# Optimization experiments

Hardware: AMD Instinct MI355X
Metric: run time of the kernel (lower is better)

The kernel has to match this reference:

```python
import jax, jax.numpy as jnp
from jax import lax
import numpy as np

IN_F, CELL, OUT_F = 1024, 1024, 1024
B, T = 128, 256


def setup_inputs() -> dict:
    key = jax.random.key(0)
    ks = jax.random.split(key, 12)
    s_gate = 1.0 / np.sqrt(IN_F + CELL)
    s_cls = 1.0 / np.sqrt(CELL)
    d = {
        "x": jax.random.normal(ks[0], (B, T, IN_F), jnp.float32),
        "Wf": jax.random.normal(ks[1], (CELL + IN_F, CELL), jnp.float32) * s_gate,
        "bf": jax.random.normal(ks[2], (CELL,), jnp.float32) * s_gate,
        "Wi1": jax.random.normal(ks[3], (CELL + IN_F, CELL), jnp.float32) * s_gate,
        "bi1": jax.random.normal(ks[4], (CELL,), jnp.float32) * s_gate,
        "Wi2": jax.random.normal(ks[5], (CELL + IN_F, CELL), jnp.float32) * s_gate,
        "bi2": jax.random.normal(ks[6], (CELL,), jnp.float32) * s_gate,
        "Wo": jax.random.normal(ks[7], (CELL + IN_F, CELL), jnp.float32) * s_gate,
        "bo": jax.random.normal(ks[8], (CELL,), jnp.float32) * s_gate,
        "Wc": jax.random.normal(ks[9], (CELL, OUT_F), jnp.float32) * s_cls,
        "bc": jax.random.normal(ks[10], (OUT_F,), jnp.float32) * s_cls,
    }
    return d


def reference(x, Wf, bf, Wi1, bi1, Wi2, bi2, Wo, bo, Wc, bc):
    # x: [B, T, IN_F]
    Bsz, Tlen, _ = x.shape
    H = Wf.shape[1]
    xt = jnp.transpose(x, (1, 0, 2))  # [T, B, IN_F], matches x.permute(1,0,2)

    def step(cell, x_i):
        # concat order matches torch.cat((cell_state, x[i]), dim=2)
        inp = jnp.concatenate([cell, x_i], axis=-1)  # [B, H + IN_F]
        f = jax.nn.sigmoid(inp @ Wf + bf)
        cell1 = cell * f
        i1 = jax.nn.sigmoid(inp @ Wi1 + bi1)
        i2 = jnp.tanh(inp @ Wi2 + bi2)
        cell2 = cell1 + i1 * i2
        o1 = jax.nn.sigmoid(inp @ Wo + bo)
        h = o1 * jnp.tanh(cell2)
        out = h @ Wc + bc  # [B, OUT_F]
        return cell2, out

    c0 = jnp.zeros((Bsz, H), x.dtype)
    c_final, outs = lax.scan(step, c0, xt)  # outs: [T, B, OUT_F]
    output_sequence = jnp.transpose(outs, (1, 0, 2))  # [B, T, OUT_F]
    return output_sequence, c_final[None, :, :]  # cell_state kept as [1, B, H]
```

## Files before the change

### kernel.cpp

```cpp
#include <hip/hip_runtime.h>
#include <cstdint>
#include <cstddef>

#define DEVINL __device__ __forceinline__

typedef __attribute__((ext_vector_type(8))) short bf16x8;
typedef __attribute__((ext_vector_type(4))) float f32x4;
typedef __attribute__((ext_vector_type(4))) unsigned short u16x4;
typedef __attribute__((ext_vector_type(4))) unsigned int u32x4;

static constexpr size_t OFF_XB   = 0;
static constexpr size_t OFF_WHT  = OFF_XB  + (size_t)32768*1024*2;
static constexpr size_t OFF_WXT  = OFF_WHT + (size_t)4096*1024*2;
static constexpr size_t OFF_WCT  = OFF_WXT + (size_t)4096*1024*2;
static constexpr size_t OFF_BIAS = OFF_WCT + (size_t)1024*1024*2;
static constexpr size_t OFF_XW   = OFF_BIAS + 4096*4;
static constexpr size_t OFF_H    = OFF_XW  + (size_t)32768*4096*2;
static constexpr size_t OFF_CB   = OFF_H   + (size_t)32768*1024*2;
static constexpr size_t OFF_BAR  = OFF_CB  + (size_t)2*128*1024*2;
static constexpr size_t WS_NEEDED = OFF_BAR + 32768;

DEVINL unsigned short f2b(float f) {
  union { float f; unsigned u; } v; v.f = f;
  unsigned r = (v.u + 0x7FFFu + ((v.u >> 16) & 1u)) >> 16;
  return (unsigned short)r;
}
DEVINL float b2f(unsigned short h) {
  union { unsigned u; float f; } v; v.u = ((unsigned)h) << 16;
  return v.f;
}
DEVINL float sigmoidf_(float x) { return 1.0f / (1.0f + __expf(-x)); }
DEVINL float tanhf_(float x) { float e = __expf(2.0f * x); return 1.0f - 2.0f / (e + 1.0f); }
DEVINL f32x4 MFMA(bf16x8 a, bf16x8 b, f32x4 c) {
  return __builtin_amdgcn_mfma_f32_16x16x32_bf16(a, b, c, 0, 0, 0);
}
DEVINL void gload16(const void* g, void* l) {
  __builtin_amdgcn_global_load_lds(
      (const __attribute__((address_space(1))) void*)g,
      (__attribute__((address_space(3))) void*)l, 16, 0, 0);
}

__global__ void cvt_x_kernel(const float* __restrict__ x, unsigned short* __restrict__ xb) {
  size_t i = ((size_t)blockIdx.x * 256 + threadIdx.x) * 4;
  float4 v = *(const float4*)(x + i);
  u16x4 o; o.x = f2b(v.x); o.y = f2b(v.y); o.z = f2b(v.z); o.w = f2b(v.w);
  *(u16x4*)(xb + i) = o;
}

__global__ __launch_bounds__(256)
void cvt_w_kernel(const float* __restrict__ Wf, const float* __restrict__ Wi1,
                  const float* __restrict__ Wi2, const float* __restrict__ Wo,
                  unsigned short* __restrict__ WhT, unsigned short* __restrict__ WxT) {
  __shared__ float tile[64][65];
  const int bid = blockIdx.x;
  const int g  = bid & 3;
  const int kt = (bid >> 2) & 15;
  const int jt = bid >> 6;
  const float* W = (g == 0) ? Wf : (g == 1) ? Wi1 : (g == 2) ? Wi2 : Wo;
  const int tid = threadIdx.x;
  const int jj  = tid & 63;
  const int kr  = tid >> 6;

  for (int h = 0; h < 2; ++h) {
    const float* Wb = W + (size_t)(h ? 1024 : 0) * 1024;
#pragma unroll
    for (int i = 0; i < 16; ++i) {
      int kl = i * 4 + kr;
      tile[kl][jj] = Wb[(size_t)(kt * 64 + kl) * 1024 + jt * 64 + jj];
    }
    __syncthreads();
    unsigned short* Out = h ? WxT : WhT;
    unsigned short* op  = Out + (size_t)(4 * (jt * 64 + jj) + g) * 1024 + kt * 64 + kr * 16;
#pragma unroll
    for (int q = 0; q < 4; ++q) {
      u16x4 v;
#pragma unroll
      for (int e = 0; e < 4; ++e)
        ((unsigned short*)&v)[e] = f2b(tile[kr * 16 + q * 4 + e][jj]);
      *(u16x4*)(op + q * 4) = v;
    }
    __syncthreads();
  }
}

__global__ void bias_kernel(const float* __restrict__ bf_, const float* __restrict__ bi1,
                            const float* __restrict__ bi2, const float* __restrict__ bo,
                            float* __restrict__ biasAll) {
  int gc = blockIdx.x * 256 + threadIdx.x;
  int j = gc >> 2, g = gc & 3;
  const float* bb = (g == 0) ? bf_ : (g == 1) ? bi1 : (g == 2) ? bi2 : bo;
  biasAll[gc] = bb[j];
}

__global__ void cvt_wc_kernel(const float* __restrict__ Wc, unsigned short* __restrict__ WcT) {
  int idx = blockIdx.x * 256 + threadIdx.x;
  int k = idx & 1023, n = idx >> 10;
  WcT[idx] = f2b(Wc[(size_t)k * 1024 + n]);
}

template<bool OUT_F32>
__global__ __launch_bounds__(512, 2)
void gemm_bt(const unsigned short* __restrict__ A,
             const unsigned short* __restrict__ Bt,
             const float* __restrict__ bias,
             void* __restrict__ C,
             int M, int N, int K) {
  __shared__ char sT[4][32768];
  const int tid  = threadIdx.x;
  const int lane = tid & 63;
  const int wid  = tid >> 6;
  const int wm   = (wid >> 2) * 128;
  const int wn   = (wid & 3) * 64;

  const int nwg = gridDim.x * gridDim.y;
  const int lin = blockIdx.y * gridDim.x + blockIdx.x;
  const int cpx = nwg >> 3;
  const int swz = (lin & 7) * cpx + (lin >> 3);
  const int m0  = (swz / gridDim.x) * 256;
  const int n0  = (swz % gridDim.x) * 256;

  const int nt = K >> 5;

  f32x4 acc[8][4];
#pragma unroll
  for (int i = 0; i < 8; ++i)
#pragma unroll
    for (int j = 0; j < 4; ++j) acc[i][j] = (f32x4){0.f, 0.f, 0.f, 0.f};

  auto stageA = [&](int kt, int buf) {
#pragma unroll
    for (int l = 0; l < 2; ++l) {
      int s = l * 512 + tid;
      int r = s >> 2, c = s & 3;
      int cg = c ^ ((r >> 1) & 3);
      gload16(A + (size_t)(m0 + r) * K + kt * 32 + cg * 8, sT[buf] + s * 16);
    }
  };
  auto stageB = [&](int kt, int buf) {
#pragma unroll
    for (int l = 0; l < 2; ++l) {
      int s = l * 512 + tid;
      int r = s >> 2, c = s & 3;
      int cg = c ^ ((r >> 1) & 3);
      gload16(Bt + (size_t)(n0 + r) * K + kt * 32 + cg * 8, sT[buf] + 16384 + s * 16);
    }
  };

  stageA(0, 0); stageB(0, 0);
  stageA(1, 1); stageB(1, 1);
  stageA(2, 2); stageB(2, 2);
  asm volatile("s_waitcnt vmcnt(8)" ::: "memory");
  __builtin_amdgcn_s_barrier();

  const int ch = lane >> 4;

#pragma unroll 1
  for (int g = 0; g < nt; ++g) {
    const int rb = g & 3;
    const char* ab = sT[rb];
    const char* bb = sT[rb] + 16384;

    bf16x8 bv[4], av[4];
#pragma unroll
    for (int ni = 0; ni < 4; ++ni) {
      int col = wn + ni * 16 + (lane & 15);
      bv[ni] = *(const bf16x8*)(bb + col * 64 + ((ch ^ ((col >> 1) & 3)) << 4));
    }
#pragma unroll
    for (int mi = 0; mi < 4; ++mi) {
      int row = wm + mi * 16 + (lane & 15);
      av[mi] = *(const bf16x8*)(ab + row * 64 + ((ch ^ ((row >> 1) & 3)) << 4));
    }
    if (g + 3 < nt) stageA(g + 3, (g + 3) & 3);
    __builtin_amdgcn_s_barrier();
    __builtin_amdgcn_s_setprio(1);
#pragma unroll
    for (int mi = 0; mi < 4; ++mi)
#pragma unroll
      for (int ni = 0; ni < 4; ++ni)
        acc[mi][ni] = MFMA(av[mi], bv[ni], acc[mi][ni]);
    __builtin_amdgcn_s_setprio(0);
    __builtin_amdgcn_s_barrier();

#pragma unroll
    for (int mi = 0; mi < 4; ++mi) {
      int row = wm + 64 + mi * 16 + (lane & 15);
      av[mi] = *(const bf16x8*)(ab + row * 64 + ((ch ^ ((row >> 1) & 3)) << 4));
    }
    if (g + 3 < nt) stageB(g + 3, (g + 3) & 3);
    __builtin_amdgcn_s_barrier();
    __builtin_amdgcn_s_setprio(1);
#pragma unroll
    for (int mi = 0; mi < 4; ++mi)
#pragma unroll
      for (int ni = 0; ni < 4; ++ni)
        acc[mi + 4][ni] = MFMA(av[mi], bv[ni], acc[mi + 4][ni]);
    __builtin_amdgcn_s_setprio(0);

    if (g <= nt - 4)      asm volatile("s_waitcnt vmcnt(8)" ::: "memory");
    else if (g == nt - 3) asm volatile("s_waitcnt vmcnt(4)" ::: "memory");
    else if (g == nt - 2) asm volatile("s_waitcnt vmcnt(0)" ::: "memory");
    __builtin_amdgcn_s_barrier();
  }

#pragma unroll
  for (int mi = 0; mi < 8; ++mi)
#pragma unroll
    for (int ni = 0; ni < 4; ++ni)
#pragma unroll
      for (int r = 0; r < 4; ++r) {
        int row = m0 + wm + mi * 16 + (lane >> 4) * 4 + r;
        int col = n0 + wn + ni * 16 + (lane & 15);
        float v = acc[mi][ni][r] + bias[col];
        if (OUT_F32) ((float*)C)[(size_t)row * N + col] = v;
        else ((unsigned short*)C)[(size_t)row * N + col] = f2b(v);
      }
}

__global__ __launch_bounds__(512, 2)
void lstm_persist(const unsigned short* __restrict__ WhT,
                  const unsigned short* __restrict__ XW,
                  unsigned short* __restrict__ H,
                  unsigned short* __restrict__ cB0,
                  unsigned short* __restrict__ cB1,
                  float* __restrict__ cellOut,
                  unsigned* __restrict__ bar) {
  __shared__ __align__(16) char  sA[16 * 2064];
  __shared__ __align__(16) float sP[16 * 132];

  const int tid  = threadIdx.x;
  const int lane = tid & 63;
  const int nh   = tid >> 6;
  const int wgid = blockIdx.x;
  const int mq   = wgid & 7;
  const int cs   = wgid >> 3;
  const int sg   = cs >> 2;

  unsigned* qc   = bar + mq * 64;
  unsigned* qf   = bar + 512 + mq * 64;
  unsigned* gcnt = bar + 1024 + (mq * 8 + sg) * 64;

  const int r0 = lane & 15;
  const int ch = lane >> 4;

  bf16x8 bfr[32];
  {
    const unsigned short* bp = WhT + (size_t)(cs * 128 + nh * 16 + r0) * 1024 + ch * 8;
#pragma unroll
    for (int ks = 0; ks < 32; ++ks)
      bfr[ks] = *(const volatile bf16x8*)(bp + ks * 32);
  }

  const int b_local = (tid & 255) >> 4;
  const int jp      = (tid & 15) * 2;
  const int browg   = mq * 16 + b_local;
  float cf0 = 0.f, cf1 = 0.f;

  const unsigned short* xwp = XW + (size_t)browg * 256 * 4096 + cs * 128 + jp * 4;
  unsigned* c0p = (unsigned*)(cB0 + (size_t)browg * 1024 + cs * 32 + jp);
  unsigned* c1p = (unsigned*)(cB1 + (size_t)browg * 1024 + cs * 32 + jp);
  unsigned short* hp = H + (size_t)browg * 256 * 1024 + cs * 32 + jp;

  const int strow = tid >> 7;
  const int stcc  = tid & 127;

  for (int t = 0; t < 256; ++t) {
    const unsigned short* cinq = ((t & 1) ? cB1 : cB0) + (size_t)mq * 16 * 1024;

    bf16x8 xw;
    if (tid < 256) xw = *(const bf16x8*)(xwp + (size_t)t * 4096);

    u32x4 st[4];
#pragma unroll
    for (int it = 0; it < 4; ++it) {
      const void* p = cinq + (size_t)(it * 4 + strow) * 1024 + stcc * 8;
      asm volatile("global_load_dwordx4 %0, %1, off sc0 sc1"
                   : "=&v"(st[it]) : "v"(p) : "memory");
    }
    asm volatile("s_waitcnt vmcnt(0)" ::: "memory");
    __builtin_amdgcn_sched_barrier(0);
#pragma unroll
    for (int it = 0; it < 4; ++it) {
      int r = it * 4 + strow;
      *(u32x4*)&sA[r * 2064 + stcc * 16] = st[it];
    }
    __syncthreads();

    f32x4 acc = (f32x4){0.f, 0.f, 0.f, 0.f};
#pragma unroll
    for (int ks = 0; ks < 32; ++ks) {
      bf16x8 a0 = *(const bf16x8*)&sA[r0 * 2064 + (ch + ks * 4) * 16];
      acc = MFMA(a0, bfr[ks], acc);
    }

#pragma unroll
    for (int rr = 0; rr < 4; ++rr)
      sP[(ch * 4 + rr) * 132 + nh * 16 + r0] = acc[rr];
    __syncthreads();

    if (tid < 256) {
      float4 g0 = *(const float4*)&sP[b_local * 132 + jp * 4];
      float4 g1 = *(const float4*)&sP[b_local * 132 + jp * 4 + 4];

      float c2a, c2b, ha, hb;
      {
        float pf = g0.x + b2f((unsigned short)xw[0]);
        float pi = g0.y + b2f((unsigned short)xw[1]);
        float pg = g0.z + b2f((unsigned short)xw[2]);
        float po = g0.w + b2f((unsigned short)xw[3]);
        float f = sigmoidf_(pf), i1 = sigmoidf_(pi), gg = tanhf_(pg), o = sigmoidf_(po);
        c2a = cf0 * f + i1 * gg; cf0 = c2a; ha = o * tanhf_(c2a);
      }
      {
        float pf = g1.x + b2f((unsigned short)xw[4]);
        float pi = g1.y + b2f((unsigned short)xw[5]);
        float pg = g1.z + b2f((unsigned short)xw[6]);
        float po = g1.w + b2f((unsigned short)xw[7]);
        float f = sigmoidf_(pf), i1 = sigmoidf_(pi), gg = tanhf_(pg), o = sigmoidf_(po);
        c2b = cf1 * f + i1 * gg; cf1 = c2b; hb = o * tanhf_(c2b);
      }

      unsigned cw = (unsigned)f2b(c2a) | ((unsigned)f2b(c2b) << 16);
      __hip_atomic_store((t & 1) ? c0p : c1p, cw,
                         __ATOMIC_RELAXED, __HIP_MEMORY_SCOPE_AGENT);
      unsigned hw = (unsigned)f2b(ha) | ((unsigned)f2b(hb) << 16);
      *(unsigned*)(hp + (size_t)t * 1024) = hw;
    }

    __syncthreads();
    if (tid == 0) {
      unsigned tgt1 = 4u * (unsigned)(t + 1);
      unsigned tgt2 = 8u * (unsigned)(t + 1);
      unsigned n = __hip_atomic_fetch_add(gcnt, 1u, __ATOMIC_RELAXED,
                                          __HIP_MEMORY_SCOPE_AGENT);
      if (n == tgt1 - 1u) {
        unsigned m = __hip_atomic_fetch_add(qc, 1u, __ATOMIC_RELAXED,
                                            __HIP_MEMORY_SCOPE_AGENT);
        if (m == tgt2 - 1u)
          __hip_atomic_store(qf, (unsigned)(t + 1),
                             __ATOMIC_RELAXED, __HIP_MEMORY_SCOPE_AGENT);
      }
      while (__hip_atomic_load(qf, __ATOMIC_RELAXED, __HIP_MEMORY_SCOPE_AGENT)
             < (unsigned)(t + 1))
        __builtin_amdgcn_s_sleep(1);
    }
    __syncthreads();
  }

  if (tid < 256)
    *(float2*)(cellOut + (size_t)browg * 1024 + cs * 32 + jp) = make_float2(cf0, cf1);
}

extern "C" void kernel_launch(void* const* d_in, const int* in_sizes, int n_in,
                              void* d_out, int out_size, void* d_ws, size_t ws_size,
                              hipStream_t stream) {
  const float* x   = (const float*)d_in[0];
  const float* Wf  = (const float*)d_in[1];
  const float* bfv = (const float*)d_in[2];
  const float* Wi1 = (const float*)d_in[3];
  const float* bi1 = (const float*)d_in[4];
  const float* Wi2 = (const float*)d_in[5];
  const float* bi2 = (const float*)d_in[6];
  const float* Wo  = (const float*)d_in[7];
  const float* bo  = (const float*)d_in[8];
  const float* Wc  = (const float*)d_in[9];
  const float* bc  = (const float*)d_in[10];
  float* out = (float*)d_out;

  if (ws_size < WS_NEEDED) return;

  char* ws = (char*)d_ws;
  unsigned short* xb      = (unsigned short*)(ws + OFF_XB);
  unsigned short* WhT     = (unsigned short*)(ws + OFF_WHT);
  unsigned short* WxT     = (unsigned short*)(ws + OFF_WXT);
  unsigned short* WcT     = (unsigned short*)(ws + OFF_WCT);
  float*          biasAll = (float*)(ws + OFF_BIAS);
  unsigned short* XW      = (unsigned short*)(ws + OFF_XW);
  unsigned short* H       = (unsigned short*)(ws + OFF_H);
  unsigned short* cB0     = (unsigned short*)(ws + OFF_CB);
  unsigned short* cB1     = (unsigned short*)(ws + OFF_CB + (size_t)128 * 1024 * 2);
  unsigned*       barLn   = (unsigned*)(ws + OFF_BAR);
  float*          cellOut = out + (size_t)32768 * 1024;

  hipMemsetAsync(cB0, 0, (size_t)128 * 1024 * 2, stream);
  hipMemsetAsync(barLn, 0, 32768, stream);

  cvt_x_kernel <<<32768, 256, 0, stream>>>(x, xb);
  cvt_w_kernel <<< 1024, 256, 0, stream>>>(Wf, Wi1, Wi2, Wo, WhT, WxT);
  bias_kernel  <<<   16, 256, 0, stream>>>(bfv, bi1, bi2, bo, biasAll);
  cvt_wc_kernel<<< 4096, 256, 0, stream>>>(Wc, WcT);

  gemm_bt<false><<<dim3(16, 128), 512, 0, stream>>>(xb, WxT, biasAll, XW, 32768, 4096, 1024);

  {
    void* args[] = { (void*)&WhT, (void*)&XW, (void*)&H,
                     (void*)&cB0, (void*)&cB1, (void*)&cellOut, (void*)&barLn };
    hipLaunchCooperativeKernel(lstm_persist, dim3(256), dim3(512), args, 0u, stream);
  }

  gemm_bt<true><<<dim3(4, 128), 512, 0, stream>>>(H, WcT, bc, out, 32768, 1024, 1024);
}
```

Baseline: 1.415 ms.

## Spread gate epilogue over all threads and overlap output-gate work with barrier

The elementwise gate epilogue now uses all 512 threads, one cell column each, instead of 256 threads handling two columns. Packed bf16 cell and h stores are rebuilt with lane shuffles. The output-gate and h computation and the next step's XW prefetch are moved between the barrier arrive and the spin-wait, so they run off the recurrence's critical path. This shortens the serial per-step epilogue before the cross-workgroup barrier, at the cost of extra shuffles and some register pressure.

```diff
diff --git a/kernel.cpp b/kernel.cpp
--- a/kernel.cpp
+++ b/kernel.cpp
@@ -251,24 +251,23 @@
       bfr[ks] = *(const volatile bf16x8*)(bp + ks * 32);
   }
 
-  const int b_local = (tid & 255) >> 4;
-  const int jp      = (tid & 15) * 2;
-  const int browg   = mq * 16 + b_local;
-  float cf0 = 0.f, cf1 = 0.f;
-
-  const unsigned short* xwp = XW + (size_t)browg * 256 * 4096 + cs * 128 + jp * 4;
-  unsigned* c0p = (unsigned*)(cB0 + (size_t)browg * 1024 + cs * 32 + jp);
-  unsigned* c1p = (unsigned*)(cB1 + (size_t)browg * 1024 + cs * 32 + jp);
-  unsigned short* hp = H + (size_t)browg * 256 * 1024 + cs * 32 + jp;
+  const int erow  = tid >> 5;
+  const int ecol  = tid & 31;
+  const int browg = mq * 16 + erow;
+  float cf = 0.f;
+
+  const unsigned short* xwp = XW + (size_t)browg * 256 * 4096 + cs * 128 + ecol * 4;
+  unsigned* c0p = (unsigned*)(cB0 + (size_t)browg * 1024 + cs * 32 + ecol);
+  unsigned* c1p = (unsigned*)(cB1 + (size_t)browg * 1024 + cs * 32 + ecol);
+  unsigned* hp  = (unsigned*)(H + (size_t)browg * 256 * 1024 + cs * 32 + ecol);
 
   const int strow = tid >> 7;
   const int stcc  = tid & 127;
 
+  u16x4 xw = *(const u16x4*)(xwp);
+
   for (int t = 0; t < 256; ++t) {
     const unsigned short* cinq = ((t & 1) ? cB1 : cB0) + (size_t)mq * 16 * 1024;
-
-    bf16x8 xw;
-    if (tid < 256) xw = *(const bf16x8*)(xwp + (size_t)t * 4096);
 
     u32x4 st[4];
 #pragma unroll
@@ -298,34 +297,18 @@
       sP[(ch * 4 + rr) * 132 + nh * 16 + r0] = acc[rr];
     __syncthreads();
 
-    if (tid < 256) {
-      float4 g0 = *(const float4*)&sP[b_local * 132 + jp * 4];
-      float4 g1 = *(const float4*)&sP[b_local * 132 + jp * 4 + 4];
-
-      float c2a, c2b, ha, hb;
-      {
-        float pf = g0.x + b2f((unsigned short)xw[0]);
-        float pi = g0.y + b2f((unsigned short)xw[1]);
-        float pg = g0.z + b2f((unsigned short)xw[2]);
-        float po = g0.w + b2f((unsigned short)xw[3]);
-        float f = sigmoidf_(pf), i1 = sigmoidf_(pi), gg = tanhf_(pg), o = sigmoidf_(po);
-        c2a = cf0 * f + i1 * gg; cf0 = c2a; ha = o * tanhf_(c2a);
-      }
-      {
-        float pf = g1.x + b2f((unsigned short)xw[4]);
-        float pi = g1.y + b2f((unsigned short)xw[5]);
-        float pg = g1.z + b2f((unsigned short)xw[6]);
-        float po = g1.w + b2f((unsigned short)xw[7]);
-        float f = sigmoidf_(pf), i1 = sigmoidf_(pi), gg = tanhf_(pg), o = sigmoidf_(po);
-        c2b = cf1 * f + i1 * gg; cf1 = c2b; hb = o * tanhf_(c2b);
-      }
-
-      unsigned cw = (unsigned)f2b(c2a) | ((unsigned)f2b(c2b) << 16);
-      __hip_atomic_store((t & 1) ? c0p : c1p, cw,
+    float4 g = *(const float4*)&sP[erow * 132 + ecol * 4];
+    float pf = g.x + b2f((unsigned short)xw[0]);
+    float pi = g.y + b2f((unsigned short)xw[1]);
+    float pg = g.z + b2f((unsigned short)xw[2]);
+    float f  = sigmoidf_(pf), i1 = sigmoidf_(pi), gg = tanhf_(pg);
+    float c2 = cf * f + i1 * gg; cf = c2;
+
+    unsigned cl = f2b(c2);
+    unsigned chi = __shfl_down(cl, 1);
+    if (!(lane & 1))
+      __hip_atomic_store((t & 1) ? c0p : c1p, cl | (chi << 16),
                          __ATOMIC_RELAXED, __HIP_MEMORY_SCOPE_AGENT);
-      unsigned hw = (unsigned)f2b(ha) | ((unsigned)f2b(hb) << 16);
-      *(unsigned*)(hp + (size_t)t * 1024) = hw;
-    }
 
     __syncthreads();
     if (tid == 0) {
@@ -340,6 +323,19 @@
           __hip_atomic_store(qf, (unsigned)(t + 1),
                              __ATOMIC_RELAXED, __HIP_MEMORY_SCOPE_AGENT);
       }
+    }
+
+    {
+      float po = g.w + b2f((unsigned short)xw[3]);
+      float h  = sigmoidf_(po) * tanhf_(c2);
+      unsigned hl = f2b(h);
+      unsigned hh = __shfl_down(hl, 1);
+      if (!(lane & 1))
+        *(hp + (size_t)t * 512) = hl | (hh << 16);
+    }
+    if (t < 255) xw = *(const u16x4*)(xwp + (size_t)(t + 1) * 4096);
+
+    if (tid == 0) {
       while (__hip_atomic_load(qf, __ATOMIC_RELAXED, __HIP_MEMORY_SCOPE_AGENT)
              < (unsigned)(t + 1))
         __builtin_amdgcn_s_sleep(1);
@@ -347,8 +343,7 @@
     __syncthreads();
   }
 
-  if (tid < 256)
-    *(float2*)(cellOut + (size_t)browg * 1024 + cs * 32 + jp) = make_float2(cf0, cf1);
+  cellOut[(size_t)browg * 1024 + cs * 32 + ecol] = cf;
 }
 
 extern "C" void kernel_launch(void* const* d_in, const int* in_sizes, int n_in,
```

Measured after the change: 1.337 ms (median of 2 runs). 1.06x faster.
